# Kernel tuning notes

Measured on AMD Instinct MI355X. Metric: run time of the kernel, lower is better.

## Reference

```python
import jax, jax.numpy as jnp
import numpy as np

B, S, H, NH, I = 8, 1024, 1024, 16, 4096
HD = H // NH
EPS = 1e-6
NEG = -1e9


def _glorot(key, shape):
    lim = np.sqrt(6.0 / (shape[0] + shape[1]))
    return jax.random.uniform(key, shape, jnp.float32, -lim, lim)


def setup_inputs() -> dict:
    key = jax.random.key(0)
    ks = jax.random.split(key, 8)
    return {
        "inputs": jax.random.normal(ks[0], (B, S, H), jnp.float32),
        "inputs_mask": jnp.zeros((B, S), jnp.float32),  # 1.0 marks padding
        "attn_qkvw": _glorot(ks[1], (H, 3 * H)),
        "attn_qkvb": jnp.zeros((3 * H,), jnp.float32),
        "attn_ow": _glorot(ks[2], (H, H)),
        "attn_ob": jnp.zeros((H,), jnp.float32),
        "attn_nw": jnp.ones((H,), jnp.float32),
        "attn_nb": jnp.zeros((H,), jnp.float32),
        "inter_w": _glorot(ks[3], (H, I)),
        "inter_b": jnp.zeros((I,), jnp.float32),
        "output_w": _glorot(ks[4], (I, H)),
        "output_b": jnp.zeros((H,), jnp.float32),
        "ffn_nw": jnp.ones((H,), jnp.float32),
        "ffn_nb": jnp.zeros((H,), jnp.float32),
    }


def _layer_norm(x, g, b):
    m = jnp.mean(x, axis=-1, keepdims=True)
    v = jnp.mean(jnp.square(x - m), axis=-1, keepdims=True)
    return (x - m) * jax.lax.rsqrt(v + EPS) * g + b


def reference(inputs, inputs_mask, attn_qkvw, attn_qkvb, attn_ow, attn_ob,
              attn_nw, attn_nb, inter_w, inter_b, output_w, output_b,
              ffn_nw, ffn_nb):
    # ---- self-attention block (pre-LN) ----
    res = inputs
    x = _layer_norm(inputs, attn_nw, attn_nb)
    qkv = x @ attn_qkvw + attn_qkvb                      # [B,S,3H]
    q, k, v = jnp.split(qkv, 3, axis=-1)
    q = q.reshape(B, S, NH, HD)
    k = k.reshape(B, S, NH, HD)
    v = v.reshape(B, S, NH, HD)
    scale = 1.0 / np.sqrt(HD)
    scores = jnp.einsum("bqhd,bkhd->bhqk", q, k) * scale
    scores = scores + inputs_mask[:, None, None, :] * NEG
    probs = jax.nn.softmax(scores, axis=-1)
    ctx = jnp.einsum("bhqk,bkhd->bqhd", probs, v).reshape(B, S, H)
    attn_out = ctx @ attn_ow + attn_ob
    x = res + attn_out
    # ---- FFN block (pre-LN, ReLU) ----
    res2 = x
    y = _layer_norm(x, ffn_nw, ffn_nb)
    h = jax.nn.relu(y @ inter_w + inter_b)
    return res2 + h @ output_w + output_b
```

## Files before the change

kernel.cpp:

```cpp
#include <hip/hip_runtime.h>
#include <cstdint>
#include <cstddef>

typedef _Float16 f16;
typedef _Float16 half8 __attribute__((ext_vector_type(8)));
typedef _Float16 half4v __attribute__((ext_vector_type(4)));
typedef float floatx4 __attribute__((ext_vector_type(4)));
typedef float floatx16 __attribute__((ext_vector_type(16)));

__device__ __forceinline__ floatx4 mfma16(half8 a, half8 b, floatx4 c) {
    return __builtin_amdgcn_mfma_f32_16x16x32_f16(a, b, c, 0, 0, 0);
}
__device__ __forceinline__ floatx16 mfma32(half8 a, half8 b, floatx16 c) {
    return __builtin_amdgcn_mfma_f32_32x32x16_f16(a, b, c, 0, 0, 0);
}

__device__ __forceinline__ void async16(const f16* g, f16* l) {
    __builtin_amdgcn_global_load_lds(
        (const __attribute__((address_space(1))) unsigned int*)(uintptr_t)g,
        (__attribute__((address_space(3))) unsigned int*)(uintptr_t)l,
        16, 0, 0);
}

__global__ __launch_bounds__(256)
void ln_f16_kernel(const float* __restrict__ x, const float* __restrict__ g,
                   const float* __restrict__ be, f16* __restrict__ y)
{
    int row = blockIdx.x, t = threadIdx.x;
    const float* xr = x + (size_t)row * 1024;
    float4 v = *(const float4*)(xr + t * 4);
    float s1 = v.x + v.y + v.z + v.w;
    float s2 = v.x * v.x + v.y * v.y + v.z * v.z + v.w * v.w;
    #pragma unroll
    for (int off = 32; off >= 1; off >>= 1) {
        s1 += __shfl_xor(s1, off);
        s2 += __shfl_xor(s2, off);
    }
    __shared__ float r1[4], r2[4];
    if ((t & 63) == 0) { r1[t >> 6] = s1; r2[t >> 6] = s2; }
    __syncthreads();
    s1 = r1[0] + r1[1] + r1[2] + r1[3];
    s2 = r2[0] + r2[1] + r2[2] + r2[3];
    float mean = s1 * 0.0009765625f;
    float var  = s2 * 0.0009765625f - mean * mean;
    float rs = rsqrtf(var + 1e-6f);
    float4 gv = *(const float4*)(g + t * 4);
    float4 bv = *(const float4*)(be + t * 4);
    half4v o;
    o[0] = (f16)((v.x - mean) * rs * gv.x + bv.x);
    o[1] = (f16)((v.y - mean) * rs * gv.y + bv.y);
    o[2] = (f16)((v.z - mean) * rs * gv.z + bv.z);
    o[3] = (f16)((v.w - mean) * rs * gv.w + bv.w);
    *(half4v*)(y + (size_t)row * 1024 + t * 4) = o;
}

__global__ __launch_bounds__(256)
void transpose_f16_kernel(const float* __restrict__ W, f16* __restrict__ WT,
                          int R, int C)
{
    __shared__ float tile[32][33];
    int tx = threadIdx.x & 31, ty0 = threadIdx.x >> 5;
    int r0 = blockIdx.y * 32, c0 = blockIdx.x * 32;
    #pragma unroll
    for (int i = 0; i < 4; ++i)
        tile[ty0 + i * 8][tx] = W[(size_t)(r0 + ty0 + i * 8) * C + c0 + tx];
    __syncthreads();
    #pragma unroll
    for (int i = 0; i < 4; ++i)
        WT[(size_t)(c0 + ty0 + i * 8) * R + r0 + tx] = (f16)tile[tx][ty0 + i * 8];
}

__global__ __launch_bounds__(256, 2)
void gemm_kernel(const f16* __restrict__ A, const f16* __restrict__ BT,
                 const float* __restrict__ bias, const float* __restrict__ res,
                 float* __restrict__ Cf32, int M, int N, int K)
{
    __shared__ __align__(16) f16 As[2][128 * 64];
    __shared__ __align__(16) f16 Bs[2][128 * 64];
    int m0 = blockIdx.x * 128, n0 = blockIdx.y * 128;
    int t = threadIdx.x, lane = t & 63, wave = t >> 6;
    int quad = lane >> 4, l16 = lane & 15;
    int wm = (wave & 1) * 64, wn = (wave >> 1) * 64;
    int sw = l16 & 7;
    floatx4 acc[4][4] = {};

    const f16* gA[4]; const f16* gB[4]; int oS[4];
    #pragma unroll
    for (int c = 0; c < 4; ++c) {
        int s = c * 256 + t;
        int row = s >> 3, lg = (s & 7) ^ (row & 7);
        gA[c] = A  + (size_t)(m0 + row) * K + lg * 8;
        gB[c] = BT + (size_t)(n0 + row) * K + lg * 8;
        oS[c] = (c * 256 + (t & ~63)) * 8;
    }

    #pragma unroll
    for (int c = 0; c < 4; ++c) {
        async16(gA[c], As[0] + oS[c]);
        async16(gB[c], Bs[0] + oS[c]);
    }
    __syncthreads();

    int buf = 0;
    for (int k0 = 0; k0 < K; k0 += 64) {
        int kn = k0 + 64;
        if (kn < K) {
            #pragma unroll
            for (int c = 0; c < 4; ++c) {
                async16(gA[c] + kn, As[buf ^ 1] + oS[c]);
                async16(gB[c] + kn, Bs[buf ^ 1] + oS[c]);
            }
        }
        #pragma unroll
        for (int ks = 0; ks < 2; ++ks) {
            int ca = (ks * 4 + quad) ^ sw;
            half8 a[4], b[4];
            #pragma unroll
            for (int i = 0; i < 4; ++i) {
                a[i] = *(const half8*)(As[buf] + (wm + i * 16 + l16) * 64 + ca * 8);
                b[i] = *(const half8*)(Bs[buf] + (wn + i * 16 + l16) * 64 + ca * 8);
            }
            #pragma unroll
            for (int i = 0; i < 4; ++i)
                #pragma unroll
                for (int j = 0; j < 4; ++j)
                    acc[i][j] = mfma16(a[i], b[j], acc[i][j]);
        }
        __syncthreads();
        buf ^= 1;
    }

    #pragma unroll
    for (int j = 0; j < 4; ++j) {
        int col = n0 + wn + j * 16 + l16;
        float bv = bias[col];
        #pragma unroll
        for (int i = 0; i < 4; ++i) {
            int rowb = m0 + wm + i * 16 + quad * 4;
            #pragma unroll
            for (int r = 0; r < 4; ++r) {
                float v = acc[i][j][r] + bv;
                size_t idx = (size_t)(rowb + r) * N + col;
                Cf32[idx] = v + res[idx];
            }
        }
    }
}

template<int MODE>
__global__ __launch_bounds__(256, 2)
void gemm_big_kernel(const f16* __restrict__ A, const f16* __restrict__ BT,
                     const float* __restrict__ bias, f16* __restrict__ Cf16,
                     f16* __restrict__ qb, f16* __restrict__ kb, f16* __restrict__ vb,
                     int M, int N, int K)
{
    __shared__ __align__(16) f16 As[2][256 * 32];
    __shared__ __align__(16) f16 Bs[2][128 * 32];
    int m0 = blockIdx.x * 256, n0 = blockIdx.y * 128;
    int t = threadIdx.x, lane = t & 63, wave = t >> 6;
    int l32 = lane & 31, kg = lane >> 5;
    int swz = (l32 ^ (l32 >> 2) ^ (l32 >> 4)) & 3;
    floatx16 acc[2][4];
    #pragma unroll
    for (int mi = 0; mi < 2; ++mi)
        #pragma unroll
        for (int jn = 0; jn < 4; ++jn)
            #pragma unroll
            for (int r = 0; r < 16; ++r) acc[mi][jn][r] = 0.f;

    const f16* gA[4]; int oA[4];
    #pragma unroll
    for (int c = 0; c < 4; ++c) {
        int s = c * 256 + t;
        int row = s >> 2, phys = s & 3;
        int lg = phys ^ ((row ^ (row >> 2) ^ (row >> 4)) & 3);
        gA[c] = A + (size_t)(m0 + row) * K + lg * 8;
        oA[c] = (c * 256 + (t & ~63)) * 8;
    }
    const f16* gB[2]; int oB[2];
    #pragma unroll
    for (int c = 0; c < 2; ++c) {
        int s = c * 256 + t;
        int row = s >> 2, phys = s & 3;
        int lg = phys ^ ((row ^ (row >> 2) ^ (row >> 4)) & 3);
        gB[c] = BT + (size_t)(n0 + row) * K + lg * 8;
        oB[c] = (c * 256 + (t & ~63)) * 8;
    }

    #pragma unroll
    for (int c = 0; c < 4; ++c) async16(gA[c], As[0] + oA[c]);
    #pragma unroll
    for (int c = 0; c < 2; ++c) async16(gB[c], Bs[0] + oB[c]);
    __syncthreads();

    int buf = 0;
    for (int k0 = 0; k0 < K; k0 += 32) {
        int kn = k0 + 32;
        if (kn < K) {
            #pragma unroll
            for (int c = 0; c < 4; ++c) async16(gA[c] + kn, As[buf ^ 1] + oA[c]);
            #pragma unroll
            for (int c = 0; c < 2; ++c) async16(gB[c] + kn, Bs[buf ^ 1] + oB[c]);
        }
        #pragma unroll
        for (int ss = 0; ss < 2; ++ss) {
            int cb = ss * 2 + kg;
            half8 a[2], b[4];
            #pragma unroll
            for (int mi = 0; mi < 2; ++mi) {
                int ca = (cb ^ swz ^ (mi * 2));
                a[mi] = *(const half8*)(As[buf] + (wave * 64 + mi * 32 + l32) * 32 + ca * 8);
            }
            #pragma unroll
            for (int jn = 0; jn < 4; ++jn) {
                int ca = (cb ^ swz ^ ((jn & 1) * 2));
                b[jn] = *(const half8*)(Bs[buf] + (jn * 32 + l32) * 32 + ca * 8);
            }
            #pragma unroll
            for (int mi = 0; mi < 2; ++mi)
                #pragma unroll
                for (int jn = 0; jn < 4; ++jn)
                    acc[mi][jn] = mfma32(a[mi], b[jn], acc[mi][jn]);
        }
        __syncthreads();
        buf ^= 1;
    }

    #pragma unroll
    for (int mi = 0; mi < 2; ++mi) {
        int mbase = m0 + wave * 64 + mi * 32 + 4 * kg;
        #pragma unroll
        for (int jn = 0; jn < 4; ++jn) {
            int col = n0 + jn * 32 + l32;
            float bv = bias[col];
            if (MODE == 1) {
                #pragma unroll
                for (int reg = 0; reg < 16; ++reg) {
                    int row = mbase + (reg & 3) + 8 * (reg >> 2);
                    Cf16[(size_t)row * N + col] = (f16)fmaxf(acc[mi][jn][reg] + bv, 0.f);
                }
            } else {
                int part = col >> 10;
                int h = (col >> 6) & 15;
                int d = col & 63;
                if (part == 2) {
                    #pragma unroll
                    for (int rb = 0; rb < 4; ++rb) {
                        int m = mbase + 8 * rb;
                        int bb = m >> 10, s = m & 1023;
                        size_t bh = (size_t)bb * 16 + h;
                        half4v pv;
                        #pragma unroll
                        for (int r = 0; r < 4; ++r) pv[r] = (f16)(acc[mi][jn][rb * 4 + r] + bv);
                        *(half4v*)(vb + (bh * 64 + d) * 1024 + s) = pv;
                    }
                } else {
                    f16* dst0 = part == 0 ? qb : kb;
                    #pragma unroll
                    for (int reg = 0; reg < 16; ++reg) {
                        int m = mbase + (reg & 3) + 8 * (reg >> 2);
                        int bb = m >> 10, s = m & 1023;
                        size_t bh = (size_t)bb * 16 + h;
                        dst0[(bh * 1024 + s) * 64 + d] = (f16)(acc[mi][jn][reg] + bv);
                    }
                }
            }
        }
    }
}

__global__ __launch_bounds__(256)
void attn_kernel(const f16* __restrict__ qb, const f16* __restrict__ kb,
                 const f16* __restrict__ vb, const float* __restrict__ mask,
                 f16* __restrict__ ctx)
{
    const int S = 1024;
    int qt = blockIdx.x, h = blockIdx.y, b = blockIdx.z;
    size_t bh = (size_t)b * 16 + h;
    int t = threadIdx.x, lane = t & 63, wv = t >> 6;
    int quad = lane >> 4, l16 = lane & 15;
    int sw = l16 & 7;

    __shared__ __align__(16) f16 Ks[2][64 * 64];
    __shared__ __align__(16) f16 Vs[2][64 * 64];
    __shared__ __align__(16) f16 Ps[4][16 * 40];

    int q0 = qt * 64 + wv * 16;
    const f16* qrow = qb + (bh * 1024 + q0 + l16) * 64;
    half8 aq0 = *(const half8*)(qrow + quad * 8);
    half8 aq1 = *(const half8*)(qrow + 32 + quad * 8);

    floatx4 o[4] = {};
    float lsum[4] = {0.f, 0.f, 0.f, 0.f};
    const float scale = 0.125f;
    const float* mrow = mask + b * S;

    const f16* pK[2]; const f16* pV[2]; int oS[2];
    #pragma unroll
    for (int c = 0; c < 2; ++c) {
        int s = c * 256 + t;
        int row = s >> 3, lg = (s & 7) ^ (row & 7);
        pK[c] = kb + (bh * 1024 + row) * 64 + lg * 8;
        pV[c] = vb + (bh * 64 + row) * 1024 + lg * 8;
        oS[c] = (c * 256 + (t & ~63)) * 8;
    }

    #pragma unroll
    for (int c = 0; c < 2; ++c) {
        async16(pK[c], Ks[0] + oS[c]);
        async16(pV[c], Vs[0] + oS[c]);
    }
    __syncthreads();

    int buf = 0;
    for (int kc = 0; kc < S; kc += 64) {
        int kn = kc + 64;
        if (kn < S) {
            #pragma unroll
            for (int c = 0; c < 2; ++c) {
                async16(pK[c] + (size_t)kn * 64, Ks[buf ^ 1] + oS[c]);
                async16(pV[c] + kn,              Vs[buf ^ 1] + oS[c]);
            }
        }

        floatx4 sf[4];
        #pragma unroll
        for (int cg = 0; cg < 4; ++cg) {
            const f16* kr = Ks[buf] + (cg * 16 + l16) * 64;
            int c0 = quad ^ sw;
            half8 b0 = *(const half8*)(kr + c0 * 8);
            half8 b1 = *(const half8*)(kr + (c0 ^ 4) * 8);
            floatx4 z = {};
            sf[cg] = mfma16(aq1, b1, mfma16(aq0, b0, z));
        }
        #pragma unroll
        for (int cg = 0; cg < 4; ++cg) {
            float mk = mrow[kc + cg * 16 + l16] * (-1e9f);
            #pragma unroll
            for (int r = 0; r < 4; ++r) {
                float e = __expf(sf[cg][r] * scale + mk);
                lsum[r] += e;
                Ps[wv][(quad * 4 + r) * 40 + cg * 16 + l16] = (f16)e;
            }
        }
        half8 ap0 = *(const half8*)(Ps[wv] + l16 * 40 + quad * 8);
        half8 ap1 = *(const half8*)(Ps[wv] + l16 * 40 + 32 + quad * 8);
        #pragma unroll
        for (int td = 0; td < 4; ++td) {
            const f16* vr = Vs[buf] + (td * 16 + l16) * 64;
            int c0 = quad ^ sw;
            half8 bv0 = *(const half8*)(vr + c0 * 8);
            half8 bv1 = *(const half8*)(vr + (c0 ^ 4) * 8);
            o[td] = mfma16(ap0, bv0, o[td]);
            o[td] = mfma16(ap1, bv1, o[td]);
        }
        __syncthreads();
        buf ^= 1;
    }

    #pragma unroll
    for (int r = 0; r < 4; ++r) {
        float s = lsum[r];
        s += __shfl_xor(s, 1); s += __shfl_xor(s, 2);
        s += __shfl_xor(s, 4); s += __shfl_xor(s, 8);
        lsum[r] = 1.f / s;
    }
    #pragma unroll
    for (int td = 0; td < 4; ++td)
        #pragma unroll
        for (int r = 0; r < 4; ++r)
            ctx[((size_t)b * 1024 + q0 + quad * 4 + r) * 1024 + h * 64 + td * 16 + l16]
                = (f16)(o[td][r] * lsum[r]);
}

extern "C" void kernel_launch(void* const* d_in, const int* in_sizes, int n_in,
                              void* d_out, int out_size, void* d_ws, size_t ws_size,
                              hipStream_t stream)
{
    const float* inputs = (const float*)d_in[0];
    const float* mask   = (const float*)d_in[1];
    const float* qkvw   = (const float*)d_in[2];
    const float* qkvb   = (const float*)d_in[3];
    const float* ow     = (const float*)d_in[4];
    const float* ob     = (const float*)d_in[5];
    const float* anw    = (const float*)d_in[6];
    const float* anb    = (const float*)d_in[7];
    const float* iw     = (const float*)d_in[8];
    const float* ib     = (const float*)d_in[9];
    const float* outw   = (const float*)d_in[10];
    const float* outb   = (const float*)d_in[11];
    const float* fnw    = (const float*)d_in[12];
    const float* fnb    = (const float*)d_in[13];
    float* out = (float*)d_out;

    const int M = 8192;
    uint8_t* ws = (uint8_t*)d_ws;
    f16* wT_qkv = (f16*)(ws + 0);
    f16* wT_o   = (f16*)(ws + 6291456);
    f16* wT_i   = (f16*)(ws + 8388608);
    f16* wT_out = (f16*)(ws + 16777216);
    f16* xln    = (f16*)(ws + 25165824);
    float* x1   = (float*)(ws + 41943040);
    f16* qbuf   = (f16*)(ws + 75497472);
    f16* kbuf   = (f16*)(ws + 92274688);
    f16* vbuf   = (f16*)(ws + 109051904);
    f16* ctx    = (f16*)(ws + 125829120);
    f16* hbuf   = (f16*)(ws + 75497472);

    transpose_f16_kernel<<<dim3(96, 32),  256, 0, stream>>>(qkvw, wT_qkv, 1024, 3072);
    transpose_f16_kernel<<<dim3(32, 32),  256, 0, stream>>>(ow,   wT_o,   1024, 1024);
    transpose_f16_kernel<<<dim3(128, 32), 256, 0, stream>>>(iw,   wT_i,   1024, 4096);
    transpose_f16_kernel<<<dim3(32, 128), 256, 0, stream>>>(outw, wT_out, 4096, 1024);

    ln_f16_kernel<<<8192, 256, 0, stream>>>(inputs, anw, anb, xln);

    gemm_big_kernel<2><<<dim3(32, 24), 256, 0, stream>>>(xln, wT_qkv, qkvb,
        nullptr, qbuf, kbuf, vbuf, M, 3072, 1024);

    attn_kernel<<<dim3(16, 16, 8), 256, 0, stream>>>(qbuf, kbuf, vbuf, mask, ctx);

    gemm_kernel<<<dim3(64, 8), 256, 0, stream>>>(ctx, wT_o, ob, inputs,
        x1, M, 1024, 1024);

    ln_f16_kernel<<<8192, 256, 0, stream>>>(x1, fnw, fnb, xln);

    gemm_big_kernel<1><<<dim3(32, 32), 256, 0, stream>>>(xln, wT_i, ib,
        hbuf, nullptr, nullptr, nullptr, M, 4096, 1024);

    gemm_kernel<<<dim3(64, 8), 256, 0, stream>>>(hbuf, wT_out, outb, x1,
        out, M, 1024, 4096);
}
```

Before: 464.5 us.

## Process two query groups per attention block to reuse K/V tiles

```diff
diff --git a/kernel.cpp b/kernel.cpp
--- a/kernel.cpp
+++ b/kernel.cpp
@@ -285,14 +285,22 @@
     __shared__ __align__(16) f16 Vs[2][64 * 64];
     __shared__ __align__(16) f16 Ps[4][16 * 40];
 
-    int q0 = qt * 64 + wv * 16;
-    const f16* qrow = qb + (bh * 1024 + q0 + l16) * 64;
-    half8 aq0 = *(const half8*)(qrow + quad * 8);
-    half8 aq1 = *(const half8*)(qrow + 32 + quad * 8);
-
-    floatx4 o[4] = {};
-    float lsum[4] = {0.f, 0.f, 0.f, 0.f};
-    const float scale = 0.125f;
+    int q0 = qt * 128 + wv * 16;
+    half8 aq[2][2];
+    #pragma unroll
+    for (int g = 0; g < 2; ++g) {
+        const f16* qrow = qb + (bh * 1024 + q0 + g * 64 + l16) * 64;
+        aq[g][0] = *(const half8*)(qrow + quad * 8);
+        aq[g][1] = *(const half8*)(qrow + 32 + quad * 8);
+        #pragma unroll
+        for (int i = 0; i < 8; ++i) {
+            aq[g][0][i] = (f16)(aq[g][0][i] * (f16)0.125);
+            aq[g][1][i] = (f16)(aq[g][1][i] * (f16)0.125);
+        }
+    }
+
+    floatx4 o[2][4] = {};
+    float lsum[2][4] = {};
     const float* mrow = mask + b * S;
 
     const f16* pK[2]; const f16* pV[2]; int oS[2];
@@ -323,54 +331,67 @@
             }
         }
 
-        floatx4 sf[4];
+        floatx4 sf[2][4];
         #pragma unroll
         for (int cg = 0; cg < 4; ++cg) {
             const f16* kr = Ks[buf] + (cg * 16 + l16) * 64;
             int c0 = quad ^ sw;
             half8 b0 = *(const half8*)(kr + c0 * 8);
             half8 b1 = *(const half8*)(kr + (c0 ^ 4) * 8);
-            floatx4 z = {};
-            sf[cg] = mfma16(aq1, b1, mfma16(aq0, b0, z));
-        }
-        #pragma unroll
-        for (int cg = 0; cg < 4; ++cg) {
-            float mk = mrow[kc + cg * 16 + l16] * (-1e9f);
-            #pragma unroll
-            for (int r = 0; r < 4; ++r) {
-                float e = __expf(sf[cg][r] * scale + mk);
-                lsum[r] += e;
-                Ps[wv][(quad * 4 + r) * 40 + cg * 16 + l16] = (f16)e;
-            }
-        }
-        half8 ap0 = *(const half8*)(Ps[wv] + l16 * 40 + quad * 8);
-        half8 ap1 = *(const half8*)(Ps[wv] + l16 * 40 + 32 + quad * 8);
-        #pragma unroll
-        for (int td = 0; td < 4; ++td) {
-            const f16* vr = Vs[buf] + (td * 16 + l16) * 64;
-            int c0 = quad ^ sw;
-            half8 bv0 = *(const half8*)(vr + c0 * 8);
-            half8 bv1 = *(const half8*)(vr + (c0 ^ 4) * 8);
-            o[td] = mfma16(ap0, bv0, o[td]);
-            o[td] = mfma16(ap1, bv1, o[td]);
+            #pragma unroll
+            for (int g = 0; g < 2; ++g) {
+                floatx4 z = {};
+                sf[g][cg] = mfma16(aq[g][1], b1, mfma16(aq[g][0], b0, z));
+            }
+        }
+        float mkv[4];
+        #pragma unroll
+        for (int cg = 0; cg < 4; ++cg)
+            mkv[cg] = mrow[kc + cg * 16 + l16] * (-1e9f);
+
+        #pragma unroll
+        for (int g = 0; g < 2; ++g) {
+            #pragma unroll
+            for (int cg = 0; cg < 4; ++cg) {
+                #pragma unroll
+                for (int r = 0; r < 4; ++r) {
+                    float e = __expf(sf[g][cg][r] + mkv[cg]);
+                    lsum[g][r] += e;
+                    Ps[wv][(quad * 4 + r) * 40 + cg * 16 + l16] = (f16)e;
+                }
+            }
+            half8 ap0 = *(const half8*)(Ps[wv] + l16 * 40 + quad * 8);
+            half8 ap1 = *(const half8*)(Ps[wv] + l16 * 40 + 32 + quad * 8);
+            #pragma unroll
+            for (int td = 0; td < 4; ++td) {
+                const f16* vr = Vs[buf] + (td * 16 + l16) * 64;
+                int c0 = quad ^ sw;
+                half8 bv0 = *(const half8*)(vr + c0 * 8);
+                half8 bv1 = *(const half8*)(vr + (c0 ^ 4) * 8);
+                o[g][td] = mfma16(ap0, bv0, o[g][td]);
+                o[g][td] = mfma16(ap1, bv1, o[g][td]);
+            }
         }
         __syncthreads();
         buf ^= 1;
     }
 
     #pragma unroll
-    for (int r = 0; r < 4; ++r) {
-        float s = lsum[r];
-        s += __shfl_xor(s, 1); s += __shfl_xor(s, 2);
-        s += __shfl_xor(s, 4); s += __shfl_xor(s, 8);
-        lsum[r] = 1.f / s;
-    }
-    #pragma unroll
-    for (int td = 0; td < 4; ++td)
-        #pragma unroll
-        for (int r = 0; r < 4; ++r)
-            ctx[((size_t)b * 1024 + q0 + quad * 4 + r) * 1024 + h * 64 + td * 16 + l16]
-                = (f16)(o[td][r] * lsum[r]);
+    for (int g = 0; g < 2; ++g) {
+        #pragma unroll
+        for (int r = 0; r < 4; ++r) {
+            float s = lsum[g][r];
+            s += __shfl_xor(s, 1); s += __shfl_xor(s, 2);
+            s += __shfl_xor(s, 4); s += __shfl_xor(s, 8);
+            lsum[g][r] = 1.f / s;
+        }
+        #pragma unroll
+        for (int td = 0; td < 4; ++td)
+            #pragma unroll
+            for (int r = 0; r < 4; ++r)
+                ctx[((size_t)b * 1024 + q0 + g * 64 + quad * 4 + r) * 1024
+                    + h * 64 + td * 16 + l16] = (f16)(o[g][td][r] * lsum[g][r]);
+    }
 }
 
 extern "C" void kernel_launch(void* const* d_in, const int* in_sizes, int n_in,
@@ -417,7 +438,7 @@
     gemm_big_kernel<2><<<dim3(32, 24), 256, 0, stream>>>(xln, wT_qkv, qkvb,
         nullptr, qbuf, kbuf, vbuf, M, 3072, 1024);
 
-    attn_kernel<<<dim3(16, 16, 8), 256, 0, stream>>>(qbuf, kbuf, vbuf, mask, ctx);
+    attn_kernel<<<dim3(8, 16, 8), 256, 0, stream>>>(qbuf, kbuf, vbuf, mask, ctx);
 
     gemm_kernel<<<dim3(64, 8), 256, 0, stream>>>(ctx, wT_o, ob, inputs,
         x1, M, 1024, 1024);
```

Result: slower. 489.3 us (+5.3%).
